# Kernel tuning notes

Hardware: AMD Instinct MI355X
Metric: run time of the kernel (lower is better)

The kernel has to match this reference:

```python
import jax, jax.numpy as jnp
import numpy as np

N_NODES = 100000
N_EDGES = 1600000
DIM_IN = 64
DIM_OUT = 40
K_HOPS = 3


def setup_inputs() -> dict:
    key = jax.random.key(0)
    ks = jax.random.split(key, 6)
    x = jax.random.normal(ks[0], (N_NODES, DIM_IN), dtype=jnp.float32)
    edge_index = jax.random.randint(ks[1], (2, N_EDGES), 0, N_NODES, dtype=jnp.int64)
    W_sgc = jax.random.normal(ks[2], (DIM_IN, DIM_IN), dtype=jnp.float32) * (1.0 / np.sqrt(DIM_IN))
    b_sgc = jax.random.normal(ks[3], (DIM_IN,), dtype=jnp.float32) * 0.02
    W_head = jax.random.normal(ks[4], (DIM_IN, DIM_OUT), dtype=jnp.float32) * (1.0 / np.sqrt(DIM_IN))
    b_head = jax.random.normal(ks[5], (DIM_OUT,), dtype=jnp.float32) * 0.02
    return {"x": x, "edge_index": edge_index, "W_sgc": W_sgc, "b_sgc": b_sgc,
            "W_head": W_head, "b_head": b_head}


def _sgc_forward(x, src, dst, norm, W_sgc, b_sgc, W_head, b_head):
    n = x.shape[0]
    # K-hop normalized adjacency propagation: x <- A_hat @ x, K times
    for _ in range(K_HOPS):
        x = jax.ops.segment_sum(norm[:, None] * x[src], dst, num_segments=n)
    # SGConv linear projection
    x = x @ W_sgc + b_sgc
    # dropout is identity at inference (training=False)
    # post-MP node head: Linear(dim_in -> dim_out)
    return x @ W_head + b_head


def reference(x, edge_index, W_sgc, b_sgc, W_head, b_head):
    n = x.shape[0]
    # gcn_norm with self-loops (PyG SGConv default):
    loop = jnp.arange(n, dtype=edge_index.dtype)
    src = jnp.concatenate([edge_index[0], loop])  # message source j
    dst = jnp.concatenate([edge_index[1], loop])  # message target i
    ew = jnp.ones(src.shape[0], dtype=x.dtype)
    deg = jax.ops.segment_sum(ew, dst, num_segments=n)
    dinv = jnp.where(deg > 0, jax.lax.rsqrt(deg), 0.0)
    norm = dinv[src] * dinv[dst]  # [E + N]
    return _sgc_forward(x, src, dst, norm, W_sgc, b_sgc, W_head, b_head)
```

## Files before the change

kernel.cpp:

```cpp
#include <hip/hip_runtime.h>
#include <hip/hip_bf16.h>
#include <hip/hip_fp16.h>

#define DIMI 64
#define DIMO 40
#define DLO  32
#define DHI  8

#define NBK_SHIFT 9
#define NPBK 512
#define NBKMAX 256
#define BCAP 9216
#define CHUNK 4096


__global__ void k_zero(int* __restrict__ p, int n) {
    int i = blockIdx.x * blockDim.x + threadIdx.x;
    if (i < n) p[i] = 0;
}

__global__ void k_binA(const int* __restrict__ src, const int* __restrict__ dst,
                       int* __restrict__ bcnt, int2* __restrict__ ebDS,
                       int E, int nbk) {
    __shared__ int h[NBKMAX];
    __shared__ int lb[NBKMAX];
    __shared__ int lc[NBKMAX];
    __shared__ int gb[NBKMAX];
    __shared__ int2 eb[CHUNK];
    int t = threadIdx.x;
    int e0 = blockIdx.x * CHUNK;
    int e1 = min(e0 + CHUNK, E);
    int nE = e1 - e0;
    h[t] = 0;
    __syncthreads();
    int d[CHUNK / 256], s[CHUNK / 256];
    #pragma unroll
    for (int u = 0; u < CHUNK / 256; u++) {
        int idx = e0 + t + u * 256;
        if (idx < e1) {
            d[u] = dst[idx];
            s[u] = src[idx];
            atomicAdd(&h[d[u] >> NBK_SHIFT], 1);
        }
    }
    __syncthreads();
    int orig = h[t];
    for (int o = 1; o < 256; o <<= 1) {
        int v = (t >= o) ? h[t - o] : 0;
        __syncthreads();
        h[t] += v;
        __syncthreads();
    }
    lb[t] = h[t] - orig;
    lc[t] = 0;
    gb[t] = orig ? atomicAdd(&bcnt[t], orig) : 0;
    __syncthreads();
    #pragma unroll
    for (int u = 0; u < CHUNK / 256; u++) {
        int idx = e0 + t + u * 256;
        if (idx < e1) {
            int b = d[u] >> NBK_SHIFT;
            int r = atomicAdd(&lc[b], 1);
            eb[lb[b] + r] = make_int2(d[u], s[u]);
        }
    }
    __syncthreads();
    for (int i = t; i < nE; i += 256) {
        int2 e = eb[i];
        int b = e.x >> NBK_SHIFT;
        int slot = gb[b] + (i - lb[b]);
        if (slot < BCAP) ebDS[(size_t)b * BCAP + slot] = e;
    }
}

__global__ void k_scan_bcnt(const int* __restrict__ bcnt, int* __restrict__ bbase, int nbk) {
    __shared__ int s[256];
    int t = threadIdx.x;
    int orig = (t < nbk) ? min(bcnt[t], BCAP) : 0;
    s[t] = orig;
    __syncthreads();
    for (int o = 1; o < 256; o <<= 1) {
        int v = (t >= o) ? s[t - o] : 0;
        __syncthreads();
        s[t] += v;
        __syncthreads();
    }
    if (t < nbk) bbase[t] = s[t] - orig;
}

__global__ void k_binBC(const int* __restrict__ bcnt, const int* __restrict__ bbase,
                        const int2* __restrict__ ebDS,
                        int* __restrict__ counts, int* __restrict__ off,
                        float* __restrict__ dinv, int* __restrict__ col,
                        int N) {
    __shared__ int sh[NPBK];
    __shared__ int so[NPBK];
    __shared__ int slc[NPBK];
    __shared__ int scol[BCAP];
    int b = blockIdx.x, t = threadIdx.x;
    sh[t] = 0; sh[t + 256] = 0;
    __syncthreads();
    int n = min(bcnt[b], BCAP);
    size_t base = (size_t)b * BCAP;
    for (int i = t; i < n; i += 256)
        atomicAdd(&sh[ebDS[base + i].x & (NPBK - 1)], 1);
    __syncthreads();
    so[t] = sh[t]; so[t + 256] = sh[t + 256];
    __syncthreads();
    for (int o = 1; o < NPBK; o <<= 1) {
        int v0 = (t >= o) ? sh[t - o] : 0;
        int v1 = (t + 256 >= o) ? sh[t + 256 - o] : 0;
        __syncthreads();
        sh[t] += v0; sh[t + 256] += v1;
        __syncthreads();
    }
    int gbase = bbase[b];
    int d0 = b << NBK_SHIFT;
    #pragma unroll
    for (int half = 0; half < 2; half++) {
        int j = t + half * 256;
        int orig = so[j];
        int excl = sh[j] - orig;
        int dd = d0 + j;
        if (dd < N) {
            counts[dd] = orig;
            off[dd] = gbase + excl;
            dinv[dd] = rsqrtf((float)(orig + 1));
        }
        so[j] = excl;
        slc[j] = 0;
    }
    __syncthreads();
    for (int i = t; i < n; i += 256) {
        int2 e = ebDS[base + i];
        int local = e.x & (NPBK - 1);
        int r = atomicAdd(&slc[local], 1);
        scol[so[local] + r] = e.y;
    }
    __syncthreads();
    for (int i = t; i < n; i += 256) col[gbase + i] = scol[i];
}


__global__ void k_hist(const int* __restrict__ dst, int* __restrict__ counts, int E) {
    int i = blockIdx.x * blockDim.x + threadIdx.x;
    if (i < E) atomicAdd(&counts[dst[i]], 1);
}

__global__ void k_scatter(const int* __restrict__ src, const int* __restrict__ dst,
                          const int* __restrict__ off, int* __restrict__ cursor,
                          int* __restrict__ col, int E) {
    int i = blockIdx.x * blockDim.x + threadIdx.x;
    if (i < E) {
        int d = dst[i];
        int p = off[d] + atomicAdd(&cursor[d], 1);
        col[p] = src[i];
    }
}

__global__ void k_block_sums(const int* __restrict__ counts, int* __restrict__ partial, int n) {
    __shared__ int s[256];
    int i = blockIdx.x * 256 + threadIdx.x;
    s[threadIdx.x] = (i < n) ? counts[i] : 0;
    __syncthreads();
    for (int st = 128; st > 0; st >>= 1) {
        if (threadIdx.x < st) s[threadIdx.x] += s[threadIdx.x + st];
        __syncthreads();
    }
    if (threadIdx.x == 0) partial[blockIdx.x] = s[0];
}

__global__ void k_scan_partials(int* partial, int nb) {
    __shared__ int s[1024];
    int t = threadIdx.x;
    int orig = (t < nb) ? partial[t] : 0;
    s[t] = orig;
    __syncthreads();
    for (int o = 1; o < 1024; o <<= 1) {
        int v = (t >= o) ? s[t - o] : 0;
        __syncthreads();
        s[t] += v;
        __syncthreads();
    }
    if (t < nb) partial[t] = s[t] - orig;
}

__global__ void k_scan_final(const int* __restrict__ counts, const int* __restrict__ partial,
                             int* __restrict__ off, float* __restrict__ dinv, int n) {
    __shared__ int s[256];
    int t = threadIdx.x;
    int i = blockIdx.x * 256 + t;
    int orig = (i < n) ? counts[i] : 0;
    s[t] = orig;
    __syncthreads();
    for (int o = 1; o < 256; o <<= 1) {
        int v = (t >= o) ? s[t - o] : 0;
        __syncthreads();
        s[t] += v;
        __syncthreads();
    }
    if (i < n) {
        off[i] = s[t] - orig + partial[blockIdx.x];
        dinv[i] = rsqrtf((float)(orig + 1));
    }
}


__global__ void k_wc(const float* __restrict__ Wsgc, const float* __restrict__ bsgc,
                     const float* __restrict__ Whead, const float* __restrict__ bhead,
                     float* __restrict__ Wc, float* __restrict__ bc) {
    __shared__ float sA[DIMI * DIMI];
    __shared__ float sB[DIMI * DIMO];
    int t = threadIdx.x;
    for (int i = t; i < DIMI * DIMI; i += 256) sA[i] = Wsgc[i];
    for (int i = t; i < DIMI * DIMO; i += 256) sB[i] = Whead[i];
    __syncthreads();
    for (int o = t; o < DIMI * DIMO; o += 256) {
        int k = o / DIMO, j = o % DIMO;
        float acc = 0.f;
        #pragma unroll
        for (int m = 0; m < DIMI; m++) acc += sA[k * DIMI + m] * sB[m * DIMO + j];
        Wc[o] = acc;
    }
    if (t < DIMO) {
        float acc = bhead[t];
        #pragma unroll
        for (int m = 0; m < DIMI; m++) acc += bsgc[m] * sB[m * DIMO + t];
        bc[t] = acc;
    }
}

__global__ void k_proj(const float* __restrict__ x, const float* __restrict__ Wc,
                       const float* __restrict__ dinv,
                       __half* __restrict__ yL, __half* __restrict__ yH, int N) {
    __shared__ float sX[32 * DIMI];
    __shared__ float sW[DIMI * DIMO];
    int t = threadIdx.x;
    int n0 = blockIdx.x * 32;
    for (int i = t; i < DIMI * DIMO; i += 256) sW[i] = Wc[i];
    const float4* x4 = (const float4*)x;
    float4* sX4 = (float4*)sX;
    for (int i = t; i < 32 * (DIMI / 4); i += 256) {
        int r = n0 + i / (DIMI / 4);
        sX4[i] = (r < N) ? x4[(long)r * (DIMI / 4) + (i & (DIMI / 4 - 1))]
                         : make_float4(0.f, 0.f, 0.f, 0.f);
    }
    __syncthreads();
    for (int o = t; o < 32 * DIMO; o += 256) {
        int li = o / DIMO, j = o % DIMO;
        int node = n0 + li;
        if (node < N) {
            float acc = 0.f;
            #pragma unroll
            for (int k = 0; k < DIMI; k++) acc += sX[li * DIMI + k] * sW[k * DIMO + j];
            __half v = __float2half(dinv[node] * acc);
            if (j < DLO) yL[(long)node * DLO + j] = v;
            else         yH[(long)node * DHI + (j - DLO)] = v;
        }
    }
}

__global__ void k_hop(const __half* __restrict__ xLin, const __half* __restrict__ xHin,
                      __half* __restrict__ xLout, __half* __restrict__ xHout,
                      float* __restrict__ outF,
                      const int* __restrict__ off, const int* __restrict__ counts,
                      const float* __restrict__ dinv,
                      const int* __restrict__ col,
                      const float* __restrict__ bc, int finalHop, int N) {
    int gtid = blockIdx.x * blockDim.x + threadIdx.x;
    int node = gtid >> 6;
    int lane = threadIdx.x & 63;
    if (node >= N) return;
    int l = lane < DIMO ? lane : DIMO - 1;
    const __half* base; long stride; int foff;
    if (l < DLO) { base = xLin; stride = DLO; foff = l; }
    else         { base = xHin; stride = DHI; foff = l - DLO; }
    int rs = off[node];
    int cnt = counts[node];
    int cidx = (lane < cnt) ? col[rs + lane] : node;
    float acc = __half2float(base[(long)node * stride + foff]);
    int cmain = cnt < 64 ? cnt : 64;
    int e = 0;
    for (; e + 16 <= cmain; e += 16) {
        float v[16];
        #pragma unroll
        for (int u = 0; u < 16; u++) {
            int c = __shfl(cidx, e + u, 64);
            v[u] = __half2float(base[(long)c * stride + foff]);
        }
        float s01 = (v[0] + v[1]) + (v[2] + v[3]);
        float s23 = (v[4] + v[5]) + (v[6] + v[7]);
        float s45 = (v[8] + v[9]) + (v[10] + v[11]);
        float s67 = (v[12] + v[13]) + (v[14] + v[15]);
        acc += (s01 + s23) + (s45 + s67);
    }
    for (; e + 4 <= cmain; e += 4) {
        float v[4];
        #pragma unroll
        for (int u = 0; u < 4; u++) {
            int c = __shfl(cidx, e + u, 64);
            v[u] = __half2float(base[(long)c * stride + foff]);
        }
        acc += (v[0] + v[1]) + (v[2] + v[3]);
    }
    for (; e < cmain; e++) {
        int c = __shfl(cidx, e, 64);
        acc += __half2float(base[(long)c * stride + foff]);
    }
    for (int e2 = 64; e2 < cnt; e2++) {
        int c = col[rs + e2];
        acc += __half2float(base[(long)c * stride + foff]);
    }
    float di = dinv[node];
    float scale = finalHop ? di : di * di;
    if (lane < DIMO) {
        float r = scale * acc;
        if (finalHop) {
            outF[(long)node * DIMO + lane] = r + bc[lane];
        } else {
            __half h = __float2half(r);
            if (lane < DLO) xLout[(long)node * DLO + lane] = h;
            else            xHout[(long)node * DHI + (lane - DLO)] = h;
        }
    }
}


extern "C" void kernel_launch(void* const* d_in, const int* in_sizes, int n_in,
                              void* d_out, int out_size, void* d_ws, size_t ws_size,
                              hipStream_t stream) {
    const float* x     = (const float*)d_in[0];
    const int*   ei    = (const int*)d_in[1];
    const float* Wsgc  = (const float*)d_in[2];
    const float* bsgc  = (const float*)d_in[3];
    const float* Whead = (const float*)d_in[4];
    const float* bhead = (const float*)d_in[5];
    float* out = (float*)d_out;

    const int N = in_sizes[0] / DIMI;
    const int E = in_sizes[1] / 2;
    const int* src = ei;
    const int* dst = ei + E;
    const int nbk = (N + NPBK - 1) >> NBK_SHIFT;

    char* w = (char*)d_ws;
    auto carve = [&](size_t bytes) {
        char* p = w;
        w += (bytes + 255) & ~(size_t)255;
        return p;
    };
    int*   counts  = (int*)  carve((size_t)N * 4);
    int*   cursor  = (int*)  carve((size_t)N * 4);
    int*   off     = (int*)  carve((size_t)N * 4);
    float* dinv    = (float*)carve((size_t)N * 4);
    int*   partial = (int*)  carve(1024 * 4);
    int*   col     = (int*)  carve((size_t)E * 4);
    float* Wc      = (float*)carve(DIMI * DIMO * 4);
    float* bc      = (float*)carve(DIMO * 4);
    int*   bcnt    = (int*)  carve((size_t)nbk * 4);
    int*   bbase   = (int*)  carve((size_t)nbk * 4);
    size_t lbytes  = (size_t)N * DLO * 2;
    size_t hbytes  = (size_t)N * DHI * 2;
    size_t xbytes  = lbytes + hbytes;
    size_t ebytes  = (size_t)nbk * BCAP * 8;
    size_t ubytes  = ebytes > 2 * xbytes ? ebytes : 2 * xbytes;
    char*  uni     = carve(ubytes);
    int2*   ebDS = (int2*)uni;
    __half* xLA  = (__half*)uni;
    __half* xHA  = (__half*)(uni + lbytes);
    __half* xLB  = (__half*)(uni + xbytes);
    __half* xHB  = (__half*)(uni + xbytes + lbytes);
    size_t total_need = (size_t)(w - (char*)d_ws);
    const bool useBuckets = (ws_size >= total_need) && (nbk <= NBKMAX);

    const int B = 256;
    int nbN = (N + B - 1) / B;
    int nbE = (E + B - 1) / B;

    if (useBuckets) {
        k_zero<<<(nbk + B - 1) / B, B, 0, stream>>>(bcnt, nbk);
        int nbA = (E + CHUNK - 1) / CHUNK;
        k_binA<<<nbA, B, 0, stream>>>(src, dst, bcnt, ebDS, E, nbk);
        k_scan_bcnt<<<1, 256, 0, stream>>>(bcnt, bbase, nbk);
        k_binBC<<<nbk, B, 0, stream>>>(bcnt, bbase, ebDS, counts, off, dinv, col, N);
    } else {
        k_zero<<<nbN, B, 0, stream>>>(counts, N);
        k_zero<<<nbN, B, 0, stream>>>(cursor, N);
        k_hist<<<nbE, B, 0, stream>>>(dst, counts, E);
        k_block_sums<<<nbN, B, 0, stream>>>(counts, partial, N);
        k_scan_partials<<<1, 1024, 0, stream>>>(partial, nbN);
        k_scan_final<<<nbN, B, 0, stream>>>(counts, partial, off, dinv, N);
        k_scatter<<<nbE, B, 0, stream>>>(src, dst, off, cursor, col, E);
    }

    k_wc<<<1, 256, 0, stream>>>(Wsgc, bsgc, Whead, bhead, Wc, bc);
    k_proj<<<(N + 31) / 32, 256, 0, stream>>>(x, Wc, dinv, xLA, xHA, N);

    int hopBlocks = (N * 64 + B - 1) / B;
    k_hop<<<hopBlocks, B, 0, stream>>>(xLA, xHA, xLB, xHB, out, off, counts, dinv, col, bc, 0, N);
    k_hop<<<hopBlocks, B, 0, stream>>>(xLB, xHB, xLA, xHA, out, off, counts, dinv, col, bc, 0, N);
    k_hop<<<hopBlocks, B, 0, stream>>>(xLA, xHA, xLB, xHB, out, off, counts, dinv, col, bc, 1, N);
}
```

Before: 248.8 us.

## Split hop features into narrow column slices processed by sub-wave node groups

Stores the 40 propagated fp16 features as three separate column slices (16/16/8) and runs a templated hop kernel per slice, where each wave handles several nodes (64/F lanes per node) instead of one node per 64-lane wave. The smaller per-slice arrays are meant to fit better in cache during random gathers, and packing several nodes per wave removes the 24 idle lanes of the old mapping. The cost is three times more kernel launches and re-reading the CSR indices once per slice. It also risks divergence when nodes grouped in the same wave have different degrees.

```diff
diff --git a/kernel.cpp b/kernel.cpp
--- a/kernel.cpp
+++ b/kernel.cpp
@@ -4,8 +4,9 @@
 
 #define DIMI 64
 #define DIMO 40
-#define DLO  32
-#define DHI  8
+#define F0 16
+#define F1 16
+#define F2 8
 
 #define NBK_SHIFT 9
 #define NPBK 512
@@ -232,7 +233,8 @@
 
 __global__ void k_proj(const float* __restrict__ x, const float* __restrict__ Wc,
                        const float* __restrict__ dinv,
-                       __half* __restrict__ yL, __half* __restrict__ yH, int N) {
+                       __half* __restrict__ y0, __half* __restrict__ y1,
+                       __half* __restrict__ y2, int N) {
     __shared__ float sX[32 * DIMI];
     __shared__ float sW[DIMI * DIMO];
     int t = threadIdx.x;
@@ -254,74 +256,59 @@
             #pragma unroll
             for (int k = 0; k < DIMI; k++) acc += sX[li * DIMI + k] * sW[k * DIMO + j];
             __half v = __float2half(dinv[node] * acc);
-            if (j < DLO) yL[(long)node * DLO + j] = v;
-            else         yH[(long)node * DHI + (j - DLO)] = v;
-        }
-    }
-}
-
-__global__ void k_hop(const __half* __restrict__ xLin, const __half* __restrict__ xHin,
-                      __half* __restrict__ xLout, __half* __restrict__ xHout,
-                      float* __restrict__ outF,
-                      const int* __restrict__ off, const int* __restrict__ counts,
-                      const float* __restrict__ dinv,
-                      const int* __restrict__ col,
-                      const float* __restrict__ bc, int finalHop, int N) {
-    int gtid = blockIdx.x * blockDim.x + threadIdx.x;
-    int node = gtid >> 6;
+            if (j < F0)            y0[(long)node * F0 + j] = v;
+            else if (j < F0 + F1)  y1[(long)node * F1 + (j - F0)] = v;
+            else                   y2[(long)node * F2 + (j - F0 - F1)] = v;
+        }
+    }
+}
+
+template<int F>
+__global__ void k_hop2(const __half* __restrict__ xin, __half* __restrict__ xout,
+                       float* __restrict__ outF,
+                       const int* __restrict__ off, const int* __restrict__ counts,
+                       const float* __restrict__ dinv,
+                       const int* __restrict__ col, const float* __restrict__ bc,
+                       int foff, int finalHop, int N) {
+    constexpr int G = 64 / F;
+    int wave = (blockIdx.x * blockDim.x + threadIdx.x) >> 6;
     int lane = threadIdx.x & 63;
-    if (node >= N) return;
-    int l = lane < DIMO ? lane : DIMO - 1;
-    const __half* base; long stride; int foff;
-    if (l < DLO) { base = xLin; stride = DLO; foff = l; }
-    else         { base = xHin; stride = DHI; foff = l - DLO; }
-    int rs = off[node];
-    int cnt = counts[node];
-    int cidx = (lane < cnt) ? col[rs + lane] : node;
-    float acc = __half2float(base[(long)node * stride + foff]);
-    int cmain = cnt < 64 ? cnt : 64;
-    int e = 0;
-    for (; e + 16 <= cmain; e += 16) {
-        float v[16];
-        #pragma unroll
-        for (int u = 0; u < 16; u++) {
-            int c = __shfl(cidx, e + u, 64);
-            v[u] = __half2float(base[(long)c * stride + foff]);
-        }
-        float s01 = (v[0] + v[1]) + (v[2] + v[3]);
-        float s23 = (v[4] + v[5]) + (v[6] + v[7]);
-        float s45 = (v[8] + v[9]) + (v[10] + v[11]);
-        float s67 = (v[12] + v[13]) + (v[14] + v[15]);
-        acc += (s01 + s23) + (s45 + s67);
-    }
-    for (; e + 4 <= cmain; e += 4) {
-        float v[4];
-        #pragma unroll
-        for (int u = 0; u < 4; u++) {
-            int c = __shfl(cidx, e + u, 64);
-            v[u] = __half2float(base[(long)c * stride + foff]);
-        }
-        acc += (v[0] + v[1]) + (v[2] + v[3]);
-    }
-    for (; e < cmain; e++) {
-        int c = __shfl(cidx, e, 64);
-        acc += __half2float(base[(long)c * stride + foff]);
-    }
-    for (int e2 = 64; e2 < cnt; e2++) {
-        int c = col[rs + e2];
-        acc += __half2float(base[(long)c * stride + foff]);
-    }
-    float di = dinv[node];
-    float scale = finalHop ? di : di * di;
-    if (lane < DIMO) {
-        float r = scale * acc;
-        if (finalHop) {
-            outF[(long)node * DIMO + lane] = r + bc[lane];
-        } else {
-            __half h = __float2half(r);
-            if (lane < DLO) xLout[(long)node * DLO + lane] = h;
-            else            xHout[(long)node * DHI + (lane - DLO)] = h;
-        }
+    int f = lane & (F - 1);
+    int glane = lane & ~(F - 1);
+    int node = wave * G + (lane / F);
+    bool valid = node < N;
+    int rs = 0, cnt = 0;
+    float acc = 0.f;
+    if (valid) {
+        rs = off[node];
+        cnt = counts[node];
+        acc = __half2float(xin[(long)node * F + f]);
+    }
+    for (int b = 0; b < cnt; b += F) {
+        int rem = cnt - b;
+        int cidx = (f < rem) ? col[rs + b + f] : node;
+        int m = rem < F ? rem : F;
+        int e = 0;
+        for (; e + 4 <= m; e += 4) {
+            int c0 = __shfl(cidx, glane + e + 0, 64);
+            int c1 = __shfl(cidx, glane + e + 1, 64);
+            int c2 = __shfl(cidx, glane + e + 2, 64);
+            int c3 = __shfl(cidx, glane + e + 3, 64);
+            float v0 = __half2float(xin[(long)c0 * F + f]);
+            float v1 = __half2float(xin[(long)c1 * F + f]);
+            float v2 = __half2float(xin[(long)c2 * F + f]);
+            float v3 = __half2float(xin[(long)c3 * F + f]);
+            acc += (v0 + v1) + (v2 + v3);
+        }
+        for (; e < m; e++) {
+            int c = __shfl(cidx, glane + e, 64);
+            acc += __half2float(xin[(long)c * F + f]);
+        }
+    }
+    if (valid) {
+        float di = dinv[node];
+        if (finalHop) outF[(long)node * DIMO + foff + f] = di * acc + bc[foff + f];
+        else          xout[(long)node * F + f] = __float2half(di * di * acc);
     }
 }
 
@@ -359,17 +346,17 @@
     float* bc      = (float*)carve(DIMO * 4);
     int*   bcnt    = (int*)  carve((size_t)nbk * 4);
     int*   bbase   = (int*)  carve((size_t)nbk * 4);
-    size_t lbytes  = (size_t)N * DLO * 2;
-    size_t hbytes  = (size_t)N * DHI * 2;
-    size_t xbytes  = lbytes + hbytes;
+    size_t xbytes  = (size_t)N * DIMO * 2;
     size_t ebytes  = (size_t)nbk * BCAP * 8;
     size_t ubytes  = ebytes > 2 * xbytes ? ebytes : 2 * xbytes;
     char*  uni     = carve(ubytes);
     int2*   ebDS = (int2*)uni;
-    __half* xLA  = (__half*)uni;
-    __half* xHA  = (__half*)(uni + lbytes);
-    __half* xLB  = (__half*)(uni + xbytes);
-    __half* xHB  = (__half*)(uni + xbytes + lbytes);
+    __half* A0 = (__half*)uni;
+    __half* A1 = A0 + (size_t)N * F0;
+    __half* A2 = A1 + (size_t)N * F1;
+    __half* B0 = (__half*)(uni + xbytes);
+    __half* B1 = B0 + (size_t)N * F0;
+    __half* B2 = B1 + (size_t)N * F1;
     size_t total_need = (size_t)(w - (char*)d_ws);
     const bool useBuckets = (ws_size >= total_need) && (nbk <= NBKMAX);
 
@@ -394,10 +381,17 @@
     }
 
     k_wc<<<1, 256, 0, stream>>>(Wsgc, bsgc, Whead, bhead, Wc, bc);
-    k_proj<<<(N + 31) / 32, 256, 0, stream>>>(x, Wc, dinv, xLA, xHA, N);
-
-    int hopBlocks = (N * 64 + B - 1) / B;
-    k_hop<<<hopBlocks, B, 0, stream>>>(xLA, xHA, xLB, xHB, out, off, counts, dinv, col, bc, 0, N);
-    k_hop<<<hopBlocks, B, 0, stream>>>(xLB, xHB, xLA, xHA, out, off, counts, dinv, col, bc, 0, N);
-    k_hop<<<hopBlocks, B, 0, stream>>>(xLA, xHA, xLB, xHB, out, off, counts, dinv, col, bc, 1, N);
-}
+    k_proj<<<(N + 31) / 32, 256, 0, stream>>>(x, Wc, dinv, A0, A1, A2, N);
+
+    int g16 = (N + 15) / 16;
+    int g8  = (N + 31) / 32;
+    k_hop2<16><<<g16, B, 0, stream>>>(A0, B0, out, off, counts, dinv, col, bc,  0, 0, N);
+    k_hop2<16><<<g16, B, 0, stream>>>(A1, B1, out, off, counts, dinv, col, bc, 16, 0, N);
+    k_hop2< 8><<<g8,  B, 0, stream>>>(A2, B2, out, off, counts, dinv, col, bc, 32, 0, N);
+    k_hop2<16><<<g16, B, 0, stream>>>(B0, A0, out, off, counts, dinv, col, bc,  0, 0, N);
+    k_hop2<16><<<g16, B, 0, stream>>>(B1, A1, out, off, counts, dinv, col, bc, 16, 0, N);
+    k_hop2< 8><<<g8,  B, 0, stream>>>(B2, A2, out, off, counts, dinv, col, bc, 32, 0, N);
+    k_hop2<16><<<g16, B, 0, stream>>>(A0, B0, out, off, counts, dinv, col, bc,  0, 1, N);
+    k_hop2<16><<<g16, B, 0, stream>>>(A1, B1, out, off, counts, dinv, col, bc, 16, 1, N);
+    k_hop2< 8><<<g8,  B, 0, stream>>>(A2, B2, out, off, counts, dinv, col, bc, 32, 1, N);
+}
```

New measurement: 271.0 us. 8.9% more time.

## Pack bucketed edges into one int, merge split feature arrays, thread-per-node projection

Applied to the files above, without the earlier changes.

Bucketed edges are now packed as one 32-bit word (source shifted plus local destination) instead of an int2, which halves the staging traffic between the two binning passes. The split 32+8 half-precision feature layout becomes a single 40-wide array, and the counts array is dropped in favour of an N+1 offset array. The projection kernel now uses one thread per node with register accumulators, and the small weight-combining kernel moves earlier in the stream. Packing the source into 23 bits assumes node ids stay below about 8 million, and the 40-wide rows are not aligned to 128 bytes, which may cost some gather efficiency.

```diff
diff --git a/kernel.cpp b/kernel.cpp
--- a/kernel.cpp
+++ b/kernel.cpp
@@ -4,8 +4,6 @@
 
 #define DIMI 64
 #define DIMO 40
-#define DLO  32
-#define DHI  8
 
 #define NBK_SHIFT 9
 #define NPBK 512
@@ -20,13 +18,14 @@
 }
 
 __global__ void k_binA(const int* __restrict__ src, const int* __restrict__ dst,
-                       int* __restrict__ bcnt, int2* __restrict__ ebDS,
+                       int* __restrict__ bcnt, int* __restrict__ ebP,
                        int E, int nbk) {
     __shared__ int h[NBKMAX];
     __shared__ int lb[NBKMAX];
     __shared__ int lc[NBKMAX];
     __shared__ int gb[NBKMAX];
-    __shared__ int2 eb[CHUNK];
+    __shared__ int eb[CHUNK];
+    __shared__ unsigned char ebB[CHUNK];
     int t = threadIdx.x;
     int e0 = blockIdx.x * CHUNK;
     int e1 = min(e0 + CHUNK, E);
@@ -61,15 +60,16 @@
         if (idx < e1) {
             int b = d[u] >> NBK_SHIFT;
             int r = atomicAdd(&lc[b], 1);
-            eb[lb[b] + r] = make_int2(d[u], s[u]);
+            int slot = lb[b] + r;
+            eb[slot] = (s[u] << NBK_SHIFT) | (d[u] & (NPBK - 1));
+            ebB[slot] = (unsigned char)b;
         }
     }
     __syncthreads();
     for (int i = t; i < nE; i += 256) {
-        int2 e = eb[i];
-        int b = e.x >> NBK_SHIFT;
+        int b = ebB[i];
         int slot = gb[b] + (i - lb[b]);
-        if (slot < BCAP) ebDS[(size_t)b * BCAP + slot] = e;
+        if (slot < BCAP) ebP[(size_t)b * BCAP + slot] = eb[i];
     }
 }
 
@@ -89,10 +89,9 @@
 }
 
 __global__ void k_binBC(const int* __restrict__ bcnt, const int* __restrict__ bbase,
-                        const int2* __restrict__ ebDS,
-                        int* __restrict__ counts, int* __restrict__ off,
-                        float* __restrict__ dinv, int* __restrict__ col,
-                        int N) {
+                        const int* __restrict__ ebP,
+                        int* __restrict__ off, float* __restrict__ dinv,
+                        int* __restrict__ col, int N) {
     __shared__ int sh[NPBK];
     __shared__ int so[NPBK];
     __shared__ int slc[NPBK];
@@ -103,7 +102,7 @@
     int n = min(bcnt[b], BCAP);
     size_t base = (size_t)b * BCAP;
     for (int i = t; i < n; i += 256)
-        atomicAdd(&sh[ebDS[base + i].x & (NPBK - 1)], 1);
+        atomicAdd(&sh[ebP[base + i] & (NPBK - 1)], 1);
     __syncthreads();
     so[t] = sh[t]; so[t + 256] = sh[t + 256];
     __syncthreads();
@@ -123,19 +122,19 @@
         int excl = sh[j] - orig;
         int dd = d0 + j;
         if (dd < N) {
-            counts[dd] = orig;
             off[dd] = gbase + excl;
             dinv[dd] = rsqrtf((float)(orig + 1));
         }
         so[j] = excl;
         slc[j] = 0;
     }
+    if (t == 0 && b == (int)gridDim.x - 1) off[N] = gbase + n;
     __syncthreads();
     for (int i = t; i < n; i += 256) {
-        int2 e = ebDS[base + i];
-        int local = e.x & (NPBK - 1);
+        int e = ebP[base + i];
+        int local = e & (NPBK - 1);
         int r = atomicAdd(&slc[local], 1);
-        scol[so[local] + r] = e.y;
+        scol[so[local] + r] = e >> NBK_SHIFT;
     }
     __syncthreads();
     for (int i = t; i < n; i += 256) col[gbase + i] = scol[i];
@@ -202,6 +201,7 @@
     if (i < n) {
         off[i] = s[t] - orig + partial[blockIdx.x];
         dinv[i] = rsqrtf((float)(orig + 1));
+        if (i == n - 1) off[n] = s[t] + partial[blockIdx.x];
     }
 }
 
@@ -217,68 +217,60 @@
     __syncthreads();
     for (int o = t; o < DIMI * DIMO; o += 256) {
         int k = o / DIMO, j = o % DIMO;
-        float acc = 0.f;
-        #pragma unroll
-        for (int m = 0; m < DIMI; m++) acc += sA[k * DIMI + m] * sB[m * DIMO + j];
-        Wc[o] = acc;
+        float a = 0.f;
+        #pragma unroll
+        for (int m = 0; m < DIMI; m++) a += sA[k * DIMI + m] * sB[m * DIMO + j];
+        Wc[o] = a;
     }
     if (t < DIMO) {
-        float acc = bhead[t];
-        #pragma unroll
-        for (int m = 0; m < DIMI; m++) acc += bsgc[m] * sB[m * DIMO + t];
-        bc[t] = acc;
-    }
-}
-
-__global__ void k_proj(const float* __restrict__ x, const float* __restrict__ Wc,
-                       const float* __restrict__ dinv,
-                       __half* __restrict__ yL, __half* __restrict__ yH, int N) {
-    __shared__ float sX[32 * DIMI];
+        float a = bhead[t];
+        #pragma unroll
+        for (int m = 0; m < DIMI; m++) a += bsgc[m] * sB[m * DIMO + t];
+        bc[t] = a;
+    }
+}
+
+__global__ void k_projU(const float* __restrict__ x, const float* __restrict__ Wc,
+                        const float* __restrict__ dinv, __half* __restrict__ y, int N) {
     __shared__ float sW[DIMI * DIMO];
     int t = threadIdx.x;
-    int n0 = blockIdx.x * 32;
     for (int i = t; i < DIMI * DIMO; i += 256) sW[i] = Wc[i];
-    const float4* x4 = (const float4*)x;
-    float4* sX4 = (float4*)sX;
-    for (int i = t; i < 32 * (DIMI / 4); i += 256) {
-        int r = n0 + i / (DIMI / 4);
-        sX4[i] = (r < N) ? x4[(long)r * (DIMI / 4) + (i & (DIMI / 4 - 1))]
-                         : make_float4(0.f, 0.f, 0.f, 0.f);
-    }
-    __syncthreads();
-    for (int o = t; o < 32 * DIMO; o += 256) {
-        int li = o / DIMO, j = o % DIMO;
-        int node = n0 + li;
-        if (node < N) {
-            float acc = 0.f;
-            #pragma unroll
-            for (int k = 0; k < DIMI; k++) acc += sX[li * DIMI + k] * sW[k * DIMO + j];
-            __half v = __float2half(dinv[node] * acc);
-            if (j < DLO) yL[(long)node * DLO + j] = v;
-            else         yH[(long)node * DHI + (j - DLO)] = v;
-        }
-    }
-}
-
-__global__ void k_hop(const __half* __restrict__ xLin, const __half* __restrict__ xHin,
-                      __half* __restrict__ xLout, __half* __restrict__ xHout,
+    __syncthreads();
+    int node = blockIdx.x * 256 + t;
+    if (node >= N) return;
+    float di = dinv[node];
+    const float4* xr = (const float4*)(x + (size_t)node * DIMI);
+    float acc[DIMO];
+    #pragma unroll
+    for (int j = 0; j < DIMO; j++) acc[j] = 0.f;
+    for (int k4 = 0; k4 < DIMI / 4; k4++) {
+        float4 xv = xr[k4];
+        int k = k4 * 4;
+        #pragma unroll
+        for (int j = 0; j < DIMO; j++)
+            acc[j] += xv.x * sW[k * DIMO + j] + xv.y * sW[(k + 1) * DIMO + j]
+                    + xv.z * sW[(k + 2) * DIMO + j] + xv.w * sW[(k + 3) * DIMO + j];
+    }
+    __half2* y2 = (__half2*)(y + (size_t)node * DIMO);
+    #pragma unroll
+    for (int p = 0; p < DIMO / 2; p++)
+        y2[p] = __floats2half2_rn(di * acc[2 * p], di * acc[2 * p + 1]);
+}
+
+__global__ void k_hop(const __half* __restrict__ xin, __half* __restrict__ xout,
                       float* __restrict__ outF,
-                      const int* __restrict__ off, const int* __restrict__ counts,
-                      const float* __restrict__ dinv,
-                      const int* __restrict__ col,
-                      const float* __restrict__ bc, int finalHop, int N) {
+                      const int* __restrict__ off, const float* __restrict__ dinv,
+                      const int* __restrict__ col, const float* __restrict__ bc,
+                      int finalHop, int N) {
     int gtid = blockIdx.x * blockDim.x + threadIdx.x;
     int node = gtid >> 6;
     int lane = threadIdx.x & 63;
     if (node >= N) return;
     int l = lane < DIMO ? lane : DIMO - 1;
-    const __half* base; long stride; int foff;
-    if (l < DLO) { base = xLin; stride = DLO; foff = l; }
-    else         { base = xHin; stride = DHI; foff = l - DLO; }
     int rs = off[node];
-    int cnt = counts[node];
+    int cnt = off[node + 1] - rs;
     int cidx = (lane < cnt) ? col[rs + lane] : node;
-    float acc = __half2float(base[(long)node * stride + foff]);
+    float acc = __half2float(xin[(size_t)node * DIMO + l]);
     int cmain = cnt < 64 ? cnt : 64;
     int e = 0;
     for (; e + 16 <= cmain; e += 16) {
@@ -286,7 +278,7 @@
         #pragma unroll
         for (int u = 0; u < 16; u++) {
             int c = __shfl(cidx, e + u, 64);
-            v[u] = __half2float(base[(long)c * stride + foff]);
+            v[u] = __half2float(xin[(size_t)c * DIMO + l]);
         }
         float s01 = (v[0] + v[1]) + (v[2] + v[3]);
         float s23 = (v[4] + v[5]) + (v[6] + v[7]);
@@ -299,29 +291,20 @@
         #pragma unroll
         for (int u = 0; u < 4; u++) {
             int c = __shfl(cidx, e + u, 64);
-            v[u] = __half2float(base[(long)c * stride + foff]);
+            v[u] = __half2float(xin[(size_t)c * DIMO + l]);
         }
         acc += (v[0] + v[1]) + (v[2] + v[3]);
     }
     for (; e < cmain; e++) {
         int c = __shfl(cidx, e, 64);
-        acc += __half2float(base[(long)c * stride + foff]);
-    }
-    for (int e2 = 64; e2 < cnt; e2++) {
-        int c = col[rs + e2];
-        acc += __half2float(base[(long)c * stride + foff]);
-    }
+        acc += __half2float(xin[(size_t)c * DIMO + l]);
+    }
+    for (int e2 = 64; e2 < cnt; e2++)
+        acc += __half2float(xin[(size_t)col[rs + e2] * DIMO + l]);
     float di = dinv[node];
-    float scale = finalHop ? di : di * di;
     if (lane < DIMO) {
-        float r = scale * acc;
-        if (finalHop) {
-            outF[(long)node * DIMO + lane] = r + bc[lane];
-        } else {
-            __half h = __float2half(r);
-            if (lane < DLO) xLout[(long)node * DLO + lane] = h;
-            else            xHout[(long)node * DHI + (lane - DLO)] = h;
-        }
+        if (finalHop) outF[(size_t)node * DIMO + lane] = di * acc + bc[lane];
+        else          xout[(size_t)node * DIMO + lane] = __float2half(di * di * acc);
     }
 }
 
@@ -351,7 +334,7 @@
     };
     int*   counts  = (int*)  carve((size_t)N * 4);
     int*   cursor  = (int*)  carve((size_t)N * 4);
-    int*   off     = (int*)  carve((size_t)N * 4);
+    int*   off     = (int*)  carve((size_t)(N + 1) * 4);
     float* dinv    = (float*)carve((size_t)N * 4);
     int*   partial = (int*)  carve(1024 * 4);
     int*   col     = (int*)  carve((size_t)E * 4);
@@ -359,17 +342,13 @@
     float* bc      = (float*)carve(DIMO * 4);
     int*   bcnt    = (int*)  carve((size_t)nbk * 4);
     int*   bbase   = (int*)  carve((size_t)nbk * 4);
-    size_t lbytes  = (size_t)N * DLO * 2;
-    size_t hbytes  = (size_t)N * DHI * 2;
-    size_t xbytes  = lbytes + hbytes;
-    size_t ebytes  = (size_t)nbk * BCAP * 8;
+    size_t xbytes  = (size_t)N * DIMO * 2;
+    size_t ebytes  = (size_t)nbk * BCAP * 4;
     size_t ubytes  = ebytes > 2 * xbytes ? ebytes : 2 * xbytes;
     char*  uni     = carve(ubytes);
-    int2*   ebDS = (int2*)uni;
-    __half* xLA  = (__half*)uni;
-    __half* xHA  = (__half*)(uni + lbytes);
-    __half* xLB  = (__half*)(uni + xbytes);
-    __half* xHB  = (__half*)(uni + xbytes + lbytes);
+    int*    ebP = (int*)uni;
+    __half* xA  = (__half*)uni;
+    __half* xB  = (__half*)(uni + xbytes);
     size_t total_need = (size_t)(w - (char*)d_ws);
     const bool useBuckets = (ws_size >= total_need) && (nbk <= NBKMAX);
 
@@ -377,12 +356,14 @@
     int nbN = (N + B - 1) / B;
     int nbE = (E + B - 1) / B;
 
+    k_wc<<<1, 256, 0, stream>>>(Wsgc, bsgc, Whead, bhead, Wc, bc);
+
     if (useBuckets) {
         k_zero<<<(nbk + B - 1) / B, B, 0, stream>>>(bcnt, nbk);
         int nbA = (E + CHUNK - 1) / CHUNK;
-        k_binA<<<nbA, B, 0, stream>>>(src, dst, bcnt, ebDS, E, nbk);
+        k_binA<<<nbA, B, 0, stream>>>(src, dst, bcnt, ebP, E, nbk);
         k_scan_bcnt<<<1, 256, 0, stream>>>(bcnt, bbase, nbk);
-        k_binBC<<<nbk, B, 0, stream>>>(bcnt, bbase, ebDS, counts, off, dinv, col, N);
+        k_binBC<<<nbk, B, 0, stream>>>(bcnt, bbase, ebP, off, dinv, col, N);
     } else {
         k_zero<<<nbN, B, 0, stream>>>(counts, N);
         k_zero<<<nbN, B, 0, stream>>>(cursor, N);
@@ -393,11 +374,10 @@
         k_scatter<<<nbE, B, 0, stream>>>(src, dst, off, cursor, col, E);
     }
 
-    k_wc<<<1, 256, 0, stream>>>(Wsgc, bsgc, Whead, bhead, Wc, bc);
-    k_proj<<<(N + 31) / 32, 256, 0, stream>>>(x, Wc, dinv, xLA, xHA, N);
+    k_projU<<<nbN, B, 0, stream>>>(x, Wc, dinv, xA, N);
 
     int hopBlocks = (N * 64 + B - 1) / B;
-    k_hop<<<hopBlocks, B, 0, stream>>>(xLA, xHA, xLB, xHB, out, off, counts, dinv, col, bc, 0, N);
-    k_hop<<<hopBlocks, B, 0, stream>>>(xLB, xHB, xLA, xHA, out, off, counts, dinv, col, bc, 0, N);
-    k_hop<<<hopBlocks, B, 0, stream>>>(xLA, xHA, xLB, xHB, out, off, counts, dinv, col, bc, 1, N);
-}
+    k_hop<<<hopBlocks, B, 0, stream>>>(xA, xB, out, off, dinv, col, bc, 0, N);
+    k_hop<<<hopBlocks, B, 0, stream>>>(xB, xA, out, off, dinv, col, bc, 0, N);
+    k_hop<<<hopBlocks, B, 0, stream>>>(xA, xB, out, off, dinv, col, bc, 1, N);
+}
```

New measurement: 218.9 us. -12.0%, faster.
